# Kernel optimization log

Measured on AMD Instinct MI355X. Metric: run time of the kernel, lower is better.

Reference implementation:

```python
import jax, jax.numpy as jnp
import numpy as np

N_HEAD = 16


def setup_inputs() -> dict:
    key = jax.random.key(0)
    ks = jax.random.split(key, 9)
    B, T, C = 4, 2048, 1024
    s = 1.0 / np.sqrt(C)
    x = jax.random.normal(ks[0], (B, T, C), dtype=jnp.float32)
    Wq = jax.random.normal(ks[1], (C, C), dtype=jnp.float32) * s
    bq = jnp.zeros((C,), dtype=jnp.float32)
    Wk = jax.random.normal(ks[2], (C, C), dtype=jnp.float32) * s
    bk = jnp.zeros((C,), dtype=jnp.float32)
    Wv = jax.random.normal(ks[3], (C, C), dtype=jnp.float32) * s
    bv = jnp.zeros((C,), dtype=jnp.float32)
    Wp = jax.random.normal(ks[4], (C, C), dtype=jnp.float32) * s
    bp = jnp.zeros((C,), dtype=jnp.float32)
    return {"x": x, "Wq": Wq, "bq": bq, "Wk": Wk, "bk": bk,
            "Wv": Wv, "bv": bv, "Wp": Wp, "bp": bp}


def reference(x, Wq, bq, Wk, bk, Wv, bv, Wp, bp):
    B, T, C = x.shape
    H = N_HEAD
    D = C // H
    # QKV projections, then split heads: [B, T, C] -> [B, H, T, D]
    def split_heads(t):
        return t.reshape(B, T, H, D).transpose(0, 2, 1, 3)
    q = split_heads(x @ Wq.T + bq)
    k = split_heads(x @ Wk.T + bk)
    v = split_heads(x @ Wv.T + bv)
    # NOTE: original code applies NO causal mask despite the class name.
    att = jnp.einsum('bhtd,bhsd->bhts', q, k) * (1.0 / jnp.sqrt(jnp.float32(D)))
    att = jax.nn.softmax(att, axis=-1)
    y = jnp.einsum('bhts,bhsd->bhtd', att, v)  # [B, H, T, D]
    y = y.transpose(0, 2, 1, 3).reshape(B, T, C)
    return y @ Wp.T + bp
```

## Files before the change

### kernel.cpp

```cpp
#include <hip/hip_runtime.h>
#include <hip/hip_bf16.h>

typedef float  f32x4  __attribute__((ext_vector_type(4)));
typedef short  bf16x8 __attribute__((ext_vector_type(8)));

__device__ __forceinline__ ushort f2b(float f) {
  union { float f; unsigned u; } x; x.f = f;
  unsigned r = x.u + 0x7fffu + ((x.u >> 16) & 1u);
  return (ushort)(r >> 16);
}

__device__ __forceinline__ unsigned pk2(float lo, float hi) {
  __hip_bfloat162 t = __float22bfloat162_rn(make_float2(lo, hi));
  union { __hip_bfloat162 b; unsigned u; } c; c.b = t; return c.u;
}

__device__ __forceinline__ f32x4 fzero() {
  f32x4 z; z[0] = 0.f; z[1] = 0.f; z[2] = 0.f; z[3] = 0.f; return z;
}

__device__ __forceinline__ void gld_lds16(const ushort* g, ushort* l) {
  __builtin_amdgcn_global_load_lds(g, l, 16, 0, 0);
}

__device__ __forceinline__ int vperm_s(int j64) {
  return (j64 & 0x23) | ((j64 & 0x0C) << 1) | ((j64 & 0x10) >> 2);
}

__global__ __launch_bounds__(256) void f2bf_kernel(const float* __restrict__ in,
                                                   ushort* __restrict__ out, int n4) {
  int idx = blockIdx.x * 256 + threadIdx.x;
  int stride = gridDim.x * 256;
  for (int i = idx; i < n4; i += stride) {
    float4 v = reinterpret_cast<const float4*>(in)[i];
    ushort4 o;
    o.x = f2b(v.x); o.y = f2b(v.y); o.z = f2b(v.z); o.w = f2b(v.w);
    reinterpret_cast<ushort4*>(out)[i] = o;
  }
}

__global__ __launch_bounds__(256) void f2bf_w4(
    const float* __restrict__ w0, const float* __restrict__ w1,
    const float* __restrict__ w2, const float* __restrict__ w3,
    ushort* __restrict__ out, int n4) {
  const float* src = (blockIdx.y == 0) ? w0 : (blockIdx.y == 1) ? w1
                   : (blockIdx.y == 2) ? w2 : w3;
  ushort* dst = out + (size_t)blockIdx.y * (size_t)n4 * 4;
  int idx = blockIdx.x * 256 + threadIdx.x;
  int stride = gridDim.x * 256;
  for (int i = idx; i < n4; i += stride) {
    float4 v = reinterpret_cast<const float4*>(src)[i];
    ushort4 o;
    o.x = f2b(v.x); o.y = f2b(v.y); o.z = f2b(v.z); o.w = f2b(v.w);
    reinterpret_cast<ushort4*>(dst)[i] = o;
  }
}

__global__ __launch_bounds__(256) void gemm_bt(
    const ushort* __restrict__ A,
    const ushort* __restrict__ B,
    const float*  __restrict__ bias,
    float*  __restrict__ Cf,
    ushort* __restrict__ Cb,
    int M, int N, int K, float scale) {
  __shared__ ushort As[128 * 32];
  __shared__ ushort Bs[128 * 32];
  const int tid  = threadIdx.x;
  const int lane = tid & 63;
  const int wave = tid >> 6;
  const int wr = (wave >> 1) << 6;
  const int wc = (wave & 1) << 6;
  const int fr  = lane & 15;
  const int fk8 = (lane >> 4) << 3;

  const size_t rowA = (size_t)blockIdx.y * 128;
  const size_t rowB = (size_t)blockIdx.x * 128;
  const ushort* Ag = A + rowA * K;
  const ushort* Bg = B + rowB * K;

  const int c0 = tid, c1 = tid + 256;
  const size_t a0 = (size_t)(c0 >> 2) * K + (size_t)((c0 & 3) << 3);
  const size_t a1 = (size_t)(c1 >> 2) * K + (size_t)((c1 & 3) << 3);

  f32x4 acc[4][4];
#pragma unroll
  for (int m = 0; m < 4; ++m)
#pragma unroll
    for (int n = 0; n < 4; ++n) acc[m][n] = fzero();

  for (int k0 = 0; k0 < K; k0 += 32) {
    __syncthreads();
    gld_lds16(Ag + a0 + k0, &As[wave * 512]);
    gld_lds16(Ag + a1 + k0, &As[2048 + wave * 512]);
    gld_lds16(Bg + a0 + k0, &Bs[wave * 512]);
    gld_lds16(Bg + a1 + k0, &Bs[2048 + wave * 512]);
    asm volatile("s_waitcnt vmcnt(0)" ::: "memory");
    __syncthreads();

    bf16x8 af[4], bfv[4];
#pragma unroll
    for (int m = 0; m < 4; ++m)
      af[m] = *reinterpret_cast<const bf16x8*>(&As[(wr + m * 16 + fr) * 32 + fk8]);
#pragma unroll
    for (int n = 0; n < 4; ++n)
      bfv[n] = *reinterpret_cast<const bf16x8*>(&Bs[(wc + n * 16 + fr) * 32 + fk8]);
#pragma unroll
    for (int m = 0; m < 4; ++m)
#pragma unroll
      for (int n = 0; n < 4; ++n)
        acc[m][n] = __builtin_amdgcn_mfma_f32_16x16x32_bf16(af[m], bfv[n], acc[m][n], 0, 0, 0);
  }

  const int orow = (lane >> 4) << 2;
#pragma unroll
  for (int m = 0; m < 4; ++m) {
#pragma unroll
    for (int n = 0; n < 4; ++n) {
      size_t gc = rowB + wc + n * 16 + fr;
      float bv = bias[gc];
#pragma unroll
      for (int r = 0; r < 4; ++r) {
        size_t gr = rowA + wr + m * 16 + orow + r;
        float v = (acc[m][n][r] + bv) * scale;
        if (Cf) Cf[gr * N + gc] = v;
        else    Cb[gr * N + gc] = f2b(v);
      }
    }
  }
}

__global__ __launch_bounds__(256) void gemm_bt_vt(
    const ushort* __restrict__ A,
    const ushort* __restrict__ B,
    const float*  __restrict__ bias,
    ushort* __restrict__ VbT,
    int M, int N, int K) {
  __shared__ ushort As[128 * 32];
  __shared__ ushort Bs[128 * 32];
  const int tid  = threadIdx.x;
  const int lane = tid & 63;
  const int wave = tid >> 6;
  const int wr = (wave >> 1) << 6;
  const int wc = (wave & 1) << 6;
  const int fr  = lane & 15;
  const int fk8 = (lane >> 4) << 3;

  const size_t rowA = (size_t)blockIdx.y * 128;
  const size_t rowB = (size_t)blockIdx.x * 128;
  const ushort* Ag = A + rowA * K;
  const ushort* Bg = B + rowB * K;

  const int c0 = tid, c1 = tid + 256;
  const size_t a0 = (size_t)(c0 >> 2) * K + (size_t)((c0 & 3) << 3);
  const size_t a1 = (size_t)(c1 >> 2) * K + (size_t)((c1 & 3) << 3);

  f32x4 acc[4][4];
#pragma unroll
  for (int m = 0; m < 4; ++m)
#pragma unroll
    for (int n = 0; n < 4; ++n) acc[m][n] = fzero();

  for (int k0 = 0; k0 < K; k0 += 32) {
    __syncthreads();
    gld_lds16(Ag + a0 + k0, &As[wave * 512]);
    gld_lds16(Ag + a1 + k0, &As[2048 + wave * 512]);
    gld_lds16(Bg + a0 + k0, &Bs[wave * 512]);
    gld_lds16(Bg + a1 + k0, &Bs[2048 + wave * 512]);
    asm volatile("s_waitcnt vmcnt(0)" ::: "memory");
    __syncthreads();

    bf16x8 af[4], bfv[4];
#pragma unroll
    for (int m = 0; m < 4; ++m)
      af[m] = *reinterpret_cast<const bf16x8*>(&As[(wr + m * 16 + fr) * 32 + fk8]);
#pragma unroll
    for (int n = 0; n < 4; ++n)
      bfv[n] = *reinterpret_cast<const bf16x8*>(&Bs[(wc + n * 16 + fr) * 32 + fk8]);
#pragma unroll
    for (int m = 0; m < 4; ++m)
#pragma unroll
      for (int n = 0; n < 4; ++n)
        acc[m][n] = __builtin_amdgcn_mfma_f32_16x16x32_bf16(af[m], bfv[n], acc[m][n], 0, 0, 0);
  }

  const int orow = (lane >> 4) << 2;
#pragma unroll
  for (int m = 0; m < 4; ++m) {
#pragma unroll
    for (int n = 0; n < 4; ++n) {
      size_t gc = rowB + wc + n * 16 + fr;
      float bv = bias[gc];
#pragma unroll
      for (int r = 0; r < 4; ++r) {
        int tt = (int)rowA + wr + m * 16 + orow + r;
        int b = tt >> 11, t = tt & 2047;
        size_t idx = (size_t)b * 2097152 + gc * 2048 + (size_t)((t & ~63) + vperm_s(t & 63));
        VbT[idx] = f2b(acc[m][n][r] + bv);
      }
    }
  }
}

__global__ __launch_bounds__(512) void attn_kernel(
    const ushort* __restrict__ Qb, const ushort* __restrict__ Kb,
    const ushort* __restrict__ VbT, ushort* __restrict__ Yb) {
  __shared__ ushort Ks[2][4096];
  __shared__ ushort Vs[2][4096];
  const int tid = threadIdx.x, lane = tid & 63, wave = tid >> 6;
  const int fr = lane & 15, g = lane >> 4, fk8 = g << 3;
  const int bb = blockIdx.y >> 4, h = blockIdx.y & 15;
  const size_t rowbase = (size_t)bb * 2048;
  const int cbase = h * 64;
  const ushort* Kg  = Kb  + rowbase * 1024 + cbase;
  const ushort* VgT = VbT + (size_t)bb * 2097152 + (size_t)cbase * 2048;

  const int qrow = blockIdx.x * 128 + wave * 16 + fr;
  const ushort* qptr = &Qb[(rowbase + qrow) * 1024 + cbase];
  const bf16x8 qf0 = *reinterpret_cast<const bf16x8*>(qptr + fk8);
  const bf16x8 qf1 = *reinterpret_cast<const bf16x8*>(qptr + 32 + fk8);

  const int rS = tid >> 3;
  const int wS = (tid & 7) ^ (rS & 7);
  const ushort* sK = Kg  + (size_t)rS * 1024 + (wS << 3);
  const ushort* sV = VgT + (size_t)rS * 2048 + (wS << 3);

  f32x4 yacc[4];
#pragma unroll
  for (int nb = 0; nb < 4; ++nb) yacc[nb] = fzero();
  float mrow = -__builtin_inff(), lrow = 0.f;

  gld_lds16(sK, &Ks[0][wave * 512]);
  gld_lds16(sV, &Vs[0][wave * 512]);
  asm volatile("s_waitcnt vmcnt(0)" ::: "memory");
  __syncthreads();

  for (int t = 0; t < 32; ++t) {
    const int cur = t & 1;
    if (t < 31) {
      gld_lds16(sK + (size_t)(t + 1) * 65536, &Ks[cur ^ 1][wave * 512]);
      gld_lds16(sV + (t + 1) * 64,            &Vs[cur ^ 1][wave * 512]);
    }

    f32x4 sT[4];
#pragma unroll
    for (int jb = 0; jb < 4; ++jb) {
      const int krow = jb * 16 + fr;
      const int sw = (krow & 7) << 3;
      bf16x8 kf0 = *reinterpret_cast<const bf16x8*>(&Ks[cur][krow * 64 + (fk8 ^ sw)]);
      bf16x8 kf1 = *reinterpret_cast<const bf16x8*>(&Ks[cur][krow * 64 + ((32 + fk8) ^ sw)]);
      f32x4 z = fzero();
      __builtin_amdgcn_s_setprio(1);
      z = __builtin_amdgcn_mfma_f32_16x16x32_bf16(kf0, qf0, z, 0, 0, 0);
      z = __builtin_amdgcn_mfma_f32_16x16x32_bf16(kf1, qf1, z, 0, 0, 0);
      __builtin_amdgcn_s_setprio(0);
      sT[jb] = z;
    }

    float mx = sT[0][0];
#pragma unroll
    for (int jb = 0; jb < 4; ++jb)
#pragma unroll
      for (int r = 0; r < 4; ++r) mx = fmaxf(mx, sT[jb][r]);
    mx = fmaxf(mx, __shfl_xor(mx, 16));
    mx = fmaxf(mx, __shfl_xor(mx, 32));

    if (!__all(mx <= mrow + 8.0f)) {
      const float mnew  = fmaxf(mrow, mx);
      const float alpha = __builtin_exp2f(mrow - mnew);
      lrow *= alpha;
#pragma unroll
      for (int nb = 0; nb < 4; ++nb)
#pragma unroll
        for (int r = 0; r < 4; ++r) yacc[nb][r] *= alpha;
      mrow = mnew;
    }

    float p[4][4];
    float psum = 0.f;
#pragma unroll
    for (int jb = 0; jb < 4; ++jb)
#pragma unroll
      for (int r = 0; r < 4; ++r) {
        p[jb][r] = __builtin_exp2f(sT[jb][r] - mrow);
        psum += p[jb][r];
      }
    psum += __shfl_xor(psum, 16);
    psum += __shfl_xor(psum, 32);
    lrow += psum;

    union { bf16x8 v; unsigned u[4]; } pa0, pa1;
    pa0.u[0] = pk2(p[0][0], p[0][1]); pa0.u[1] = pk2(p[0][2], p[0][3]);
    pa0.u[2] = pk2(p[1][0], p[1][1]); pa0.u[3] = pk2(p[1][2], p[1][3]);
    pa1.u[0] = pk2(p[2][0], p[2][1]); pa1.u[1] = pk2(p[2][2], p[2][3]);
    pa1.u[2] = pk2(p[3][0], p[3][1]); pa1.u[3] = pk2(p[3][2], p[3][3]);

    const int dsw = fr & 7;
#pragma unroll
    for (int nb = 0; nb < 4; ++nb) {
      const int dd = (nb * 16 + fr) * 64;
      bf16x8 vf0 = *reinterpret_cast<const bf16x8*>(&Vs[cur][dd + ((g ^ dsw) << 3)]);
      bf16x8 vf1 = *reinterpret_cast<const bf16x8*>(&Vs[cur][dd + (((4 + g) ^ dsw) << 3)]);
      __builtin_amdgcn_s_setprio(1);
      yacc[nb] = __builtin_amdgcn_mfma_f32_16x16x32_bf16(vf0, pa0.v, yacc[nb], 0, 0, 0);
      yacc[nb] = __builtin_amdgcn_mfma_f32_16x16x32_bf16(vf1, pa1.v, yacc[nb], 0, 0, 0);
      __builtin_amdgcn_s_setprio(0);
    }

    asm volatile("s_waitcnt vmcnt(0)" ::: "memory");
    __syncthreads();
  }

  const float linv = 1.0f / lrow;
  ushort* yrow = &Yb[(rowbase + qrow) * 1024 + cbase];
#pragma unroll
  for (int nb = 0; nb < 4; ++nb) {
    ushort4 o;
    o.x = f2b(yacc[nb][0] * linv);
    o.y = f2b(yacc[nb][1] * linv);
    o.z = f2b(yacc[nb][2] * linv);
    o.w = f2b(yacc[nb][3] * linv);
    *reinterpret_cast<ushort4*>(yrow + nb * 16 + (g << 2)) = o;
  }
}

extern "C" void kernel_launch(void* const* d_in, const int* in_sizes, int n_in,
                              void* d_out, int out_size, void* d_ws, size_t ws_size,
                              hipStream_t stream) {
  const float* x  = (const float*)d_in[0];
  const float* Wq = (const float*)d_in[1];
  const float* bq = (const float*)d_in[2];
  const float* Wk = (const float*)d_in[3];
  const float* bk = (const float*)d_in[4];
  const float* Wv = (const float*)d_in[5];
  const float* bv = (const float*)d_in[6];
  const float* Wp = (const float*)d_in[7];
  const float* bp = (const float*)d_in[8];
  float* out = (float*)d_out;

  const int M = 8192, C = 1024;
  const size_t MC = (size_t)M * C, CC = (size_t)C * C;
  const size_t need = (MC * 5 + CC * 4) * sizeof(ushort);
  if (ws_size < need) return;

  ushort* xb  = (ushort*)d_ws;
  ushort* wqb = xb + MC;
  ushort* wkb = wqb + CC;
  ushort* wvb = wkb + CC;
  ushort* wpb = wvb + CC;
  ushort* Qb  = wpb + CC;
  ushort* Kb  = Qb + MC;
  ushort* VbT = Kb + MC;
  ushort* Yb  = VbT + MC;

  f2bf_kernel<<<2048, 256, 0, stream>>>(x, xb, (int)(MC / 4));
  f2bf_w4<<<dim3(256, 4), 256, 0, stream>>>(Wq, Wk, Wv, Wp, wqb, (int)(CC / 4));

  const float QSCALE = 0.18033688011112042f;
  dim3 gg(8, 64);
  gemm_bt<<<gg, 256, 0, stream>>>(xb, wqb, bq, nullptr, Qb, M, C, C, QSCALE);
  gemm_bt<<<gg, 256, 0, stream>>>(xb, wkb, bk, nullptr, Kb, M, C, C, 1.0f);
  gemm_bt_vt<<<gg, 256, 0, stream>>>(xb, wvb, bv, VbT, M, C, C);

  attn_kernel<<<dim3(16, 64), 512, 0, stream>>>(Qb, Kb, VbT, Yb);

  gemm_bt<<<gg, 256, 0, stream>>>(Yb, wpb, bp, out, nullptr, M, C, C, 1.0f);
}
```

Measured before the change: 276.6 us.

## Fuse QKV GEMMs, widen attention KV tile to 128, use MFMA for row sums

Merges the three Q/K/V projection GEMMs into one launch over a concatenated weight matrix (relying on wq/wk/wv being contiguous), with the epilogue routing each column stripe to Q, K or transposed V. The attention kernel now processes 128 keys per tile instead of 64, halving the number of barriers and loop iterations while doubling LDS buffers. Row-sum of probabilities is computed with MFMA against a ones vector instead of shuffles. The aim is less launch overhead, better GPU fill, and less sync and VALU work, at the cost of more registers and LDS.

```diff
diff --git a/kernel.cpp b/kernel.cpp
--- a/kernel.cpp
+++ b/kernel.cpp
@@ -129,12 +129,12 @@
   }
 }
 
-__global__ __launch_bounds__(256) void gemm_bt_vt(
+__global__ __launch_bounds__(256) void gemm_qkv(
     const ushort* __restrict__ A,
-    const ushort* __restrict__ B,
-    const float*  __restrict__ bias,
-    ushort* __restrict__ VbT,
-    int M, int N, int K) {
+    const ushort* __restrict__ Bw,
+    const float* __restrict__ bq, const float* __restrict__ bk, const float* __restrict__ bv,
+    ushort* __restrict__ Qb, ushort* __restrict__ Kb, ushort* __restrict__ VbT,
+    float qscale) {
   __shared__ ushort As[128 * 32];
   __shared__ ushort Bs[128 * 32];
   const int tid  = threadIdx.x;
@@ -144,11 +144,12 @@
   const int wc = (wave & 1) << 6;
   const int fr  = lane & 15;
   const int fk8 = (lane >> 4) << 3;
+  const int K = 1024;
 
   const size_t rowA = (size_t)blockIdx.y * 128;
   const size_t rowB = (size_t)blockIdx.x * 128;
   const ushort* Ag = A + rowA * K;
-  const ushort* Bg = B + rowB * K;
+  const ushort* Bg = Bw + rowB * K;
 
   const int c0 = tid, c1 = tid + 256;
   const size_t a0 = (size_t)(c0 >> 2) * K + (size_t)((c0 & 3) << 3);
@@ -183,19 +184,38 @@
         acc[m][n] = __builtin_amdgcn_mfma_f32_16x16x32_bf16(af[m], bfv[n], acc[m][n], 0, 0, 0);
   }
 
+  const int stripe  = blockIdx.x >> 3;
+  const int colbase = (blockIdx.x & 7) * 128;
   const int orow = (lane >> 4) << 2;
 #pragma unroll
   for (int m = 0; m < 4; ++m) {
 #pragma unroll
     for (int n = 0; n < 4; ++n) {
-      size_t gc = rowB + wc + n * 16 + fr;
-      float bv = bias[gc];
-#pragma unroll
-      for (int r = 0; r < 4; ++r) {
-        int tt = (int)rowA + wr + m * 16 + orow + r;
-        int b = tt >> 11, t = tt & 2047;
-        size_t idx = (size_t)b * 2097152 + gc * 2048 + (size_t)((t & ~63) + vperm_s(t & 63));
-        VbT[idx] = f2b(acc[m][n][r] + bv);
+      const int gcl = colbase + wc + n * 16 + fr;
+      if (stripe == 0) {
+        const float bb_ = bq[gcl];
+#pragma unroll
+        for (int r = 0; r < 4; ++r) {
+          size_t gr = rowA + wr + m * 16 + orow + r;
+          Qb[gr * 1024 + gcl] = f2b((acc[m][n][r] + bb_) * qscale);
+        }
+      } else if (stripe == 1) {
+        const float bb_ = bk[gcl];
+#pragma unroll
+        for (int r = 0; r < 4; ++r) {
+          size_t gr = rowA + wr + m * 16 + orow + r;
+          Kb[gr * 1024 + gcl] = f2b(acc[m][n][r] + bb_);
+        }
+      } else {
+        const float bb_ = bv[gcl];
+#pragma unroll
+        for (int r = 0; r < 4; ++r) {
+          int tt = (int)rowA + wr + m * 16 + orow + r;
+          int b = tt >> 11, t = tt & 2047;
+          size_t idx = (size_t)b * 2097152 + (size_t)gcl * 2048
+                     + (size_t)((t & ~63) + vperm_s(t & 63));
+          VbT[idx] = f2b(acc[m][n][r] + bb_);
+        }
       }
     }
   }
@@ -204,8 +224,8 @@
 __global__ __launch_bounds__(512) void attn_kernel(
     const ushort* __restrict__ Qb, const ushort* __restrict__ Kb,
     const ushort* __restrict__ VbT, ushort* __restrict__ Yb) {
-  __shared__ ushort Ks[2][4096];
-  __shared__ ushort Vs[2][4096];
+  __shared__ ushort Ks[2][128 * 64];
+  __shared__ ushort Vs[2][64 * 128];
   const int tid = threadIdx.x, lane = tid & 63, wave = tid >> 6;
   const int fr = lane & 15, g = lane >> 4, fk8 = g << 3;
   const int bb = blockIdx.y >> 4, h = blockIdx.y & 15;
@@ -219,35 +239,51 @@
   const bf16x8 qf0 = *reinterpret_cast<const bf16x8*>(qptr + fk8);
   const bf16x8 qf1 = *reinterpret_cast<const bf16x8*>(qptr + 32 + fk8);
 
-  const int rS = tid >> 3;
-  const int wS = (tid & 7) ^ (rS & 7);
-  const ushort* sK = Kg  + (size_t)rS * 1024 + (wS << 3);
-  const ushort* sV = VgT + (size_t)rS * 2048 + (wS << 3);
+  const int rKa = tid >> 3;
+  const int wKa = (tid & 7) ^ (rKa & 7);
+  const ushort* sK0 = Kg + (size_t)rKa * 1024 + (wKa << 3);
+  const ushort* sK1 = Kg + (size_t)(rKa + 64) * 1024 + (wKa << 3);
+  const int dVa = tid >> 4, pVa = tid & 15;
+  const int qVa = (pVa & 8) | ((pVa & 7) ^ (dVa & 7));
+  const ushort* sV0 = VgT + (size_t)dVa * 2048 + (qVa << 3);
+  const ushort* sV1 = VgT + (size_t)(dVa + 32) * 2048 + (qVa << 3);
 
   f32x4 yacc[4];
 #pragma unroll
   for (int nb = 0; nb < 4; ++nb) yacc[nb] = fzero();
+  f32x4 zacc = fzero();
   float mrow = -__builtin_inff(), lrow = 0.f;
 
-  gld_lds16(sK, &Ks[0][wave * 512]);
-  gld_lds16(sV, &Vs[0][wave * 512]);
+  union { bf16x8 v; unsigned u[4]; } onesu;
+#pragma unroll
+  for (int i = 0; i < 4; ++i) onesu.u[i] = 0x3F803F80u;
+  const bf16x8 ones = onesu.v;
+  const int ksw = (fr & 7) << 3;
+  const int dsw = fr & 7;
+
+  gld_lds16(sK0, &Ks[0][wave * 512]);
+  gld_lds16(sK1, &Ks[0][4096 + wave * 512]);
+  gld_lds16(sV0, &Vs[0][wave * 512]);
+  gld_lds16(sV1, &Vs[0][4096 + wave * 512]);
   asm volatile("s_waitcnt vmcnt(0)" ::: "memory");
   __syncthreads();
 
-  for (int t = 0; t < 32; ++t) {
-    const int cur = t & 1;
-    if (t < 31) {
-      gld_lds16(sK + (size_t)(t + 1) * 65536, &Ks[cur ^ 1][wave * 512]);
-      gld_lds16(sV + (t + 1) * 64,            &Vs[cur ^ 1][wave * 512]);
-    }
-
-    f32x4 sT[4];
-#pragma unroll
-    for (int jb = 0; jb < 4; ++jb) {
-      const int krow = jb * 16 + fr;
-      const int sw = (krow & 7) << 3;
-      bf16x8 kf0 = *reinterpret_cast<const bf16x8*>(&Ks[cur][krow * 64 + (fk8 ^ sw)]);
-      bf16x8 kf1 = *reinterpret_cast<const bf16x8*>(&Ks[cur][krow * 64 + ((32 + fk8) ^ sw)]);
+  auto tilestep = [&](const int cur, const int t) {
+    if (t < 15) {
+      const size_t oK = (size_t)(t + 1) * 131072;
+      const int    oV = (t + 1) * 128;
+      gld_lds16(sK0 + oK, &Ks[cur ^ 1][wave * 512]);
+      gld_lds16(sK1 + oK, &Ks[cur ^ 1][4096 + wave * 512]);
+      gld_lds16(sV0 + oV, &Vs[cur ^ 1][wave * 512]);
+      gld_lds16(sV1 + oV, &Vs[cur ^ 1][4096 + wave * 512]);
+    }
+
+    f32x4 sT[8];
+#pragma unroll
+    for (int jb = 0; jb < 8; ++jb) {
+      const ushort* kb_ = &Ks[cur][(jb * 16 + fr) * 64];
+      bf16x8 kf0 = *reinterpret_cast<const bf16x8*>(kb_ + (fk8 ^ ksw));
+      bf16x8 kf1 = *reinterpret_cast<const bf16x8*>(kb_ + ((32 + fk8) ^ ksw));
       f32x4 z = fzero();
       __builtin_amdgcn_s_setprio(1);
       z = __builtin_amdgcn_mfma_f32_16x16x32_bf16(kf0, qf0, z, 0, 0, 0);
@@ -256,18 +292,20 @@
       sT[jb] = z;
     }
 
-    float mx = sT[0][0];
-#pragma unroll
-    for (int jb = 0; jb < 4; ++jb)
-#pragma unroll
-      for (int r = 0; r < 4; ++r) mx = fmaxf(mx, sT[jb][r]);
+    f32x4 m4 = sT[0];
+#pragma unroll
+    for (int jb = 1; jb < 8; ++jb)
+#pragma unroll
+      for (int r = 0; r < 4; ++r) m4[r] = fmaxf(m4[r], sT[jb][r]);
+    float mx = fmaxf(fmaxf(m4[0], m4[1]), fmaxf(m4[2], m4[3]));
     mx = fmaxf(mx, __shfl_xor(mx, 16));
     mx = fmaxf(mx, __shfl_xor(mx, 32));
 
     if (!__all(mx <= mrow + 8.0f)) {
       const float mnew  = fmaxf(mrow, mx);
       const float alpha = __builtin_exp2f(mrow - mnew);
-      lrow *= alpha;
+      lrow = (lrow + zacc[0]) * alpha;
+      zacc = fzero();
 #pragma unroll
       for (int nb = 0; nb < 4; ++nb)
 #pragma unroll
@@ -275,42 +313,55 @@
       mrow = mnew;
     }
 
-    float p[4][4];
-    float psum = 0.f;
-#pragma unroll
-    for (int jb = 0; jb < 4; ++jb)
-#pragma unroll
-      for (int r = 0; r < 4; ++r) {
+    float p[8][4];
+#pragma unroll
+    for (int jb = 0; jb < 8; ++jb)
+#pragma unroll
+      for (int r = 0; r < 4; ++r)
         p[jb][r] = __builtin_exp2f(sT[jb][r] - mrow);
-        psum += p[jb][r];
-      }
-    psum += __shfl_xor(psum, 16);
-    psum += __shfl_xor(psum, 32);
-    lrow += psum;
-
-    union { bf16x8 v; unsigned u[4]; } pa0, pa1;
-    pa0.u[0] = pk2(p[0][0], p[0][1]); pa0.u[1] = pk2(p[0][2], p[0][3]);
-    pa0.u[2] = pk2(p[1][0], p[1][1]); pa0.u[3] = pk2(p[1][2], p[1][3]);
-    pa1.u[0] = pk2(p[2][0], p[2][1]); pa1.u[1] = pk2(p[2][2], p[2][3]);
-    pa1.u[2] = pk2(p[3][0], p[3][1]); pa1.u[3] = pk2(p[3][2], p[3][3]);
-
-    const int dsw = fr & 7;
+
+    union { bf16x8 v; unsigned u[4]; } pa[4];
+#pragma unroll
+    for (int kk = 0; kk < 4; ++kk) {
+      pa[kk].u[0] = pk2(p[2 * kk][0], p[2 * kk][1]);
+      pa[kk].u[1] = pk2(p[2 * kk][2], p[2 * kk][3]);
+      pa[kk].u[2] = pk2(p[2 * kk + 1][0], p[2 * kk + 1][1]);
+      pa[kk].u[3] = pk2(p[2 * kk + 1][2], p[2 * kk + 1][3]);
+    }
+
+    __builtin_amdgcn_s_setprio(1);
+    zacc = __builtin_amdgcn_mfma_f32_16x16x32_bf16(ones, pa[0].v, zacc, 0, 0, 0);
+    zacc = __builtin_amdgcn_mfma_f32_16x16x32_bf16(ones, pa[1].v, zacc, 0, 0, 0);
+    zacc = __builtin_amdgcn_mfma_f32_16x16x32_bf16(ones, pa[2].v, zacc, 0, 0, 0);
+    zacc = __builtin_amdgcn_mfma_f32_16x16x32_bf16(ones, pa[3].v, zacc, 0, 0, 0);
+    __builtin_amdgcn_s_setprio(0);
+
 #pragma unroll
     for (int nb = 0; nb < 4; ++nb) {
-      const int dd = (nb * 16 + fr) * 64;
-      bf16x8 vf0 = *reinterpret_cast<const bf16x8*>(&Vs[cur][dd + ((g ^ dsw) << 3)]);
-      bf16x8 vf1 = *reinterpret_cast<const bf16x8*>(&Vs[cur][dd + (((4 + g) ^ dsw) << 3)]);
+      const int dd = (nb * 16 + fr) * 128;
+      const ushort* vb_ = &Vs[cur][dd];
+      bf16x8 vf0 = *reinterpret_cast<const bf16x8*>(vb_ + (((( 0 + g) & 8) | ((( 0 + g) & 7) ^ dsw)) << 3));
+      bf16x8 vf1 = *reinterpret_cast<const bf16x8*>(vb_ + (((( 4 + g) & 8) | ((( 4 + g) & 7) ^ dsw)) << 3));
+      bf16x8 vf2 = *reinterpret_cast<const bf16x8*>(vb_ + (((( 8 + g) & 8) | ((( 8 + g) & 7) ^ dsw)) << 3));
+      bf16x8 vf3 = *reinterpret_cast<const bf16x8*>(vb_ + ((((12 + g) & 8) | (((12 + g) & 7) ^ dsw)) << 3));
       __builtin_amdgcn_s_setprio(1);
-      yacc[nb] = __builtin_amdgcn_mfma_f32_16x16x32_bf16(vf0, pa0.v, yacc[nb], 0, 0, 0);
-      yacc[nb] = __builtin_amdgcn_mfma_f32_16x16x32_bf16(vf1, pa1.v, yacc[nb], 0, 0, 0);
+      yacc[nb] = __builtin_amdgcn_mfma_f32_16x16x32_bf16(vf0, pa[0].v, yacc[nb], 0, 0, 0);
+      yacc[nb] = __builtin_amdgcn_mfma_f32_16x16x32_bf16(vf1, pa[1].v, yacc[nb], 0, 0, 0);
+      yacc[nb] = __builtin_amdgcn_mfma_f32_16x16x32_bf16(vf2, pa[2].v, yacc[nb], 0, 0, 0);
+      yacc[nb] = __builtin_amdgcn_mfma_f32_16x16x32_bf16(vf3, pa[3].v, yacc[nb], 0, 0, 0);
       __builtin_amdgcn_s_setprio(0);
     }
 
     asm volatile("s_waitcnt vmcnt(0)" ::: "memory");
     __syncthreads();
-  }
-
-  const float linv = 1.0f / lrow;
+  };
+
+  for (int t = 0; t < 16; t += 2) {
+    tilestep(0, t);
+    tilestep(1, t + 1);
+  }
+
+  const float linv = 1.0f / (lrow + zacc[0]);
   ushort* yrow = &Yb[(rowbase + qrow) * 1024 + cbase];
 #pragma unroll
   for (int nb = 0; nb < 4; ++nb) {
@@ -351,17 +402,15 @@
   ushort* Kb  = Qb + MC;
   ushort* VbT = Kb + MC;
   ushort* Yb  = VbT + MC;
+  (void)wkb; (void)wvb;
 
   f2bf_kernel<<<2048, 256, 0, stream>>>(x, xb, (int)(MC / 4));
   f2bf_w4<<<dim3(256, 4), 256, 0, stream>>>(Wq, Wk, Wv, Wp, wqb, (int)(CC / 4));
 
   const float QSCALE = 0.18033688011112042f;
-  dim3 gg(8, 64);
-  gemm_bt<<<gg, 256, 0, stream>>>(xb, wqb, bq, nullptr, Qb, M, C, C, QSCALE);
-  gemm_bt<<<gg, 256, 0, stream>>>(xb, wkb, bk, nullptr, Kb, M, C, C, 1.0f);
-  gemm_bt_vt<<<gg, 256, 0, stream>>>(xb, wvb, bv, VbT, M, C, C);
+  gemm_qkv<<<dim3(24, 64), 256, 0, stream>>>(xb, wqb, bq, bk, bv, Qb, Kb, VbT, QSCALE);
 
   attn_kernel<<<dim3(16, 64), 512, 0, stream>>>(Qb, Kb, VbT, Yb);
 
-  gemm_bt<<<gg, 256, 0, stream>>>(Yb, wpb, bp, out, nullptr, M, C, C, 1.0f);
-}
+  gemm_bt<<<dim3(8, 64), 256, 0, stream>>>(Yb, wpb, bp, out, nullptr, M, C, C, 1.0f);
+}
```

New measurement: 247.9 us. 1.12x faster.
